# Performance work log

Hardware: AMD Instinct MI355X
Metric: run time of the kernel (lower is better)

## Reference

```python
import jax, jax.numpy as jnp
import numpy as np

B, S, D = 2, 1024, 1024
E, K, I = 8, 2, 1024
LIMIT = 7.0
ALPHA = 1.702


def setup_inputs() -> dict:
    key = jax.random.key(0)
    k0, k1, k2, k3 = jax.random.split(key, 4)
    return {
        "x": jax.random.normal(k0, (B, S, D), jnp.float32),
        "norm_w": jnp.ones((D,), jnp.float32),
        "gate_w": jax.random.normal(k1, (E, D), jnp.float32) / np.sqrt(D).astype(np.float32),
        "gate_b": jnp.zeros((E,), jnp.float32),
        "mlp1_w": jax.random.normal(k2, (E, 2 * I, D), jnp.float32) / np.sqrt(D).astype(np.float32),
        "mlp1_b": jnp.zeros((E, 2 * I), jnp.float32),
        "mlp2_w": jax.random.normal(k3, (E, D, I), jnp.float32) / np.sqrt(I).astype(np.float32),
        "mlp2_b": jnp.zeros((E, D), jnp.float32),
    }


def _swiglu(t, limit):
    # interleaved gate/linear split (gpt-oss style) with clamping
    glu = jnp.minimum(t[..., ::2], limit)
    lin = jnp.clip(t[..., 1::2], -limit, limit)
    return glu * jax.nn.sigmoid(ALPHA * glu) * (lin + 1.0)


def reference(x, norm_w, gate_w, gate_b, mlp1_w, mlp1_b, mlp2_w, mlp2_b):
    eps = jnp.finfo(x.dtype).eps
    # RMSNorm
    h = x * jax.lax.rsqrt(jnp.mean(x * x, axis=-1, keepdims=True) + eps) * norm_w
    flat = h.reshape(-1, D)                              # [T, D]
    # top-k gating
    logits = flat @ gate_w.T + gate_b                    # [T, E]
    vals, idx = jax.lax.top_k(logits, K)                 # sorted descending
    wts = jax.nn.softmax(vals, axis=-1)                  # [T, K]
    # per-expert SwiGLU MLP (dense over experts, identical math to per-token gather)
    t1 = jnp.einsum('td,efd->tef', flat, mlp1_w) + mlp1_b   # [T, E, 2I]
    act = _swiglu(t1, LIMIT)                                 # [T, E, I]
    y = jnp.einsum('tei,edi->ted', act, mlp2_w) + mlp2_b     # [T, E, D]
    # gather selected experts and combine
    sel = jnp.take_along_axis(y, idx[:, :, None], axis=1)    # [T, K, D]
    out = jnp.sum(sel * wts[:, :, None], axis=1).reshape(x.shape)
    return x + out
```

## Files before the change

kernel.cpp:

```cpp
#include <hip/hip_runtime.h>
#include <stdint.h>

#define TNUM 2048
#define DDIM 1024
#define NEXP 8
#define KSEL 2
#define IDIM 1024
#define TWOI 2048
#define LIMITV 7.0f
#define ALPHAV 1.702f
#define ROWT_MAX 40
#define RMSB (TNUM / 4)
#define N81 (NEXP * TWOI * DDIM / 8)
#define N82 (NEXP * DDIM * IDIM / 8)
#define G1TOT (ROWT_MAX * (TWOI / 128))
#define G2TOT (2 * ROWT_MAX * (DDIM / 128))

typedef __attribute__((ext_vector_type(8))) short bf16x8;
typedef __attribute__((ext_vector_type(4))) float f32x4;

#define VMCNT0() asm volatile("s_waitcnt vmcnt(0)" ::: "memory")
#define BARRIER() asm volatile("s_barrier" ::: "memory")

__device__ __forceinline__ unsigned short f2bf(float f) {
  unsigned u = __float_as_uint(f);
  u += 0x7FFF + ((u >> 16) & 1);
  return (unsigned short)(u >> 16);
}

__device__ __forceinline__ int4 cvt8(float4 a, float4 b) {
  union { unsigned short us[8]; int4 v; } o;
  o.us[0] = f2bf(a.x); o.us[1] = f2bf(a.y); o.us[2] = f2bf(a.z); o.us[3] = f2bf(a.w);
  o.us[4] = f2bf(b.x); o.us[5] = f2bf(b.y); o.us[6] = f2bf(b.z); o.us[7] = f2bf(b.w);
  return o.v;
}

__device__ __forceinline__ float4 ld4bf(const unsigned short* p) {
  int2 v = *(const int2*)p;
  unsigned a = (unsigned)v.x, b = (unsigned)v.y;
  float4 r;
  r.x = __uint_as_float((a & 0xFFFFu) << 16);
  r.y = __uint_as_float(a & 0xFFFF0000u);
  r.z = __uint_as_float((b & 0xFFFFu) << 16);
  r.w = __uint_as_float(b & 0xFFFF0000u);
  return r;
}

__device__ __forceinline__ void gl2lds16(const void* g, void* l) {
  __builtin_amdgcn_global_load_lds(
      (__attribute__((address_space(1))) unsigned int*)(uintptr_t)g,
      (__attribute__((address_space(3))) unsigned int*)(uintptr_t)l, 16, 0, 0);
}

__device__ __forceinline__ int xcd_swz(int bid, int total) {
  int q = total >> 3, r = total & 7;
  int xcd = bid & 7, pos = bid >> 3;
  return (xcd < r ? xcd * (q + 1) : r * (q + 1) + (xcd - r) * q) + pos;
}

__global__ __launch_bounds__(256) void k_rms_cvt(
    const float* __restrict__ x, const float* __restrict__ norm_w,
    const float* __restrict__ gate_w, const float* __restrict__ gate_b,
    const float* __restrict__ w1f, unsigned short* __restrict__ w1b,
    unsigned short* __restrict__ hb, int* __restrict__ tidx,
    float* __restrict__ twt) {
  if ((int)blockIdx.x >= RMSB) {
    int k0 = ((int)blockIdx.x - RMSB) * 1024 + (int)threadIdx.x;
    const float4* s = (const float4*)w1f;
#pragma unroll
    for (int i = 0; i < 4; ++i) {
      int k = k0 + i * 256;
      if (k < N81) ((int4*)w1b)[k] = cvt8(s[2 * k], s[2 * k + 1]);
    }
    return;
  }
  const int lane = threadIdx.x & 63;
  const int t = blockIdx.x * 4 + (threadIdx.x >> 6);

  const float4* xr  = (const float4*)x + (size_t)t * 256 + lane * 4;
  const float4* nwr = (const float4*)norm_w + lane * 4;
  const float4* gbr = (const float4*)gate_b;
  float4 xv[4], nwv[4];
#pragma unroll
  for (int i = 0; i < 4; ++i) xv[i] = xr[i];
  float4 gb0 = gbr[0], gb1 = gbr[1];
#pragma unroll
  for (int i = 0; i < 4; ++i) nwv[i] = nwr[i];

  float ss = 0.f;
#pragma unroll
  for (int i = 0; i < 4; ++i)
    ss += xv[i].x * xv[i].x + xv[i].y * xv[i].y + xv[i].z * xv[i].z + xv[i].w * xv[i].w;
#pragma unroll
  for (int m = 1; m < 64; m <<= 1) ss += __shfl_xor(ss, m);
  const float sc = rsqrtf(ss * (1.0f / DDIM) + 1.1920929e-07f);

  float4 h[4];
#pragma unroll
  for (int i = 0; i < 4; ++i) {
    h[i].x = xv[i].x * sc * nwv[i].x;
    h[i].y = xv[i].y * sc * nwv[i].y;
    h[i].z = xv[i].z * sc * nwv[i].z;
    h[i].w = xv[i].w * sc * nwv[i].w;
  }
  int4* hw = (int4*)(hb + (size_t)t * DDIM + lane * 16);
  hw[0] = cvt8(h[0], h[1]);
  hw[1] = cvt8(h[2], h[3]);

  float p[NEXP];
#pragma unroll
  for (int e = 0; e < NEXP; ++e) {
    const float4* g4 = (const float4*)gate_w + e * 256 + lane * 4;
    float4 a = g4[0], b = g4[1], c = g4[2], d = g4[3];
    p[e] = h[0].x * a.x + h[0].y * a.y + h[0].z * a.z + h[0].w * a.w
         + h[1].x * b.x + h[1].y * b.y + h[1].z * b.z + h[1].w * b.w
         + h[2].x * c.x + h[2].y * c.y + h[2].z * c.z + h[2].w * c.w
         + h[3].x * d.x + h[3].y * d.y + h[3].z * d.z + h[3].w * d.w;
  }
#pragma unroll
  for (int m = 1; m < 64; m <<= 1) {
#pragma unroll
    for (int e = 0; e < NEXP; ++e) p[e] += __shfl_xor(p[e], m);
  }
  p[0] += gb0.x; p[1] += gb0.y; p[2] += gb0.z; p[3] += gb0.w;
  p[4] += gb1.x; p[5] += gb1.y; p[6] += gb1.z; p[7] += gb1.w;

  if (lane == 0) {
    int i0 = 0; float v0 = p[0];
#pragma unroll
    for (int e = 1; e < NEXP; ++e) if (p[e] > v0) { v0 = p[e]; i0 = e; }
    int i1 = -1; float v1 = -3.4e38f;
#pragma unroll
    for (int e = 0; e < NEXP; ++e) if (e != i0 && p[e] > v1) { v1 = p[e]; i1 = e; }
    float e1 = __expf(v1 - v0);
    float w0 = 1.f / (1.f + e1);
    int2 ip; ip.x = i0; ip.y = i1;
    float2 wp; wp.x = w0; wp.y = e1 * w0;
    ((int2*)tidx)[t] = ip;
    ((float2*)twt)[t] = wp;
  }
}

__global__ __launch_bounds__(512) void k_sched(
    const int* __restrict__ tidx, int* __restrict__ meta,
    int* __restrict__ tl, int* __restrict__ rows, int* __restrict__ sof) {
  __shared__ unsigned short cnt[256][NEXP];
  __shared__ int off[NEXP];
  __shared__ int tot[NEXP];
  const int tid = threadIdx.x;
  int e_[16], rel_[16];
  if (tid < 256) {
#pragma unroll
    for (int k = 0; k < 16; ++k) e_[k] = tidx[tid * 16 + k];
#pragma unroll
    for (int k = 0; k < 16; ++k) {
      int r = 0;
#pragma unroll
      for (int j2 = 0; j2 < 16; ++j2)
        if (j2 < k) r += (e_[j2] == e_[k]) ? 1 : 0;
      rel_[k] = r;
    }
#pragma unroll
    for (int e = 0; e < NEXP; ++e) {
      int c = 0;
#pragma unroll
      for (int k = 0; k < 16; ++k) c += (e_[k] == e) ? 1 : 0;
      cnt[tid][e] = (unsigned short)c;
    }
  }
  __syncthreads();
  {
    const int we = tid >> 6, lane = tid & 63;
    int carry = 0;
#pragma unroll
    for (int chunk = 0; chunk < 4; ++chunk) {
      int i = chunk * 64 + lane;
      int c = (int)cnt[i][we];
      int s = c;
#pragma unroll
      for (int o = 1; o < 64; o <<= 1) {
        int t2 = __shfl_up(s, o);
        if (lane >= o) s += t2;
      }
      cnt[i][we] = (unsigned short)(s - c + carry);
      carry += __shfl(s, 63);
    }
    if (lane == 0) tot[we] = carry;
  }
  __syncthreads();
  if (tid == 0) {
    int acc = 0, nt = 0;
    for (int e = 0; e < NEXP; ++e) {
      meta[8 + e] = acc; off[e] = acc;
      int c = tot[e]; acc += c;
      int ntile = (c + 127) >> 7;
      for (int r = 0; r < ntile; ++r) tl[nt++] = (e << 8) | r;
    }
    meta[16] = acc;
    meta[25] = nt;
  }
  __syncthreads();
  if (tid < 256) {
#pragma unroll
    for (int k = 0; k < 16; ++k) {
      int i = tid * 16 + k;
      int e = e_[k];
      int slot = off[e] + (int)cnt[tid][e] + rel_[k];
      rows[slot] = i >> 1;
      sof[i] = slot;
    }
  }
}

__global__ __launch_bounds__(256, 4) void k_gemm1(
    const unsigned short* __restrict__ hb, const unsigned short* __restrict__ w1b,
    const float* __restrict__ mlp1_b, const int* __restrict__ meta,
    const int* __restrict__ tl, const int* __restrict__ rows,
    const float* __restrict__ w2f, unsigned short* __restrict__ w2b,
    unsigned short* __restrict__ actb) {
  const int bid = blockIdx.x;
  const int tid = threadIdx.x, lane = tid & 63, wid = tid >> 6;
  if (bid >= G1TOT) {
    int k0 = (bid - G1TOT) * 1024 + tid;
    const float4* s = (const float4*)w2f;
#pragma unroll
    for (int i = 0; i < 4; ++i) {
      int k = k0 + i * 256;
      if (k < N82) ((int4*)w2b)[k] = cvt8(s[2 * k], s[2 * k + 1]);
    }
    return;
  }
  const int nt = meta[25];
  const int total = nt * (TWOI / 128);
  if (bid >= total) return;
  const int j = xcd_swz(bid, total);
  const int ct = j / nt;
  const int tile = tl[j - ct * nt];
  const int e = tile >> 8, rt = tile & 255;
  const int offs = meta[8 + e];
  const int n_e = meta[9 + e] - offs;

  __shared__ unsigned short As[128][64];
  __shared__ unsigned short Bs[128][64];
  __shared__ int srow[128];
  if (tid < 128) srow[tid] = rows[offs + min(rt * 128 + tid, n_e - 1)];
  __syncthreads();

  const int rloc = tid >> 3;
  const int csw  = (((tid & 7) ^ (rloc & 7)) << 3);
  const unsigned short* gA[4];
  const unsigned short* gB[4];
  const unsigned short* w1e = w1b + (size_t)e * TWOI * DDIM;
#pragma unroll
  for (int jj = 0; jj < 4; ++jj) {
    gA[jj] = hb + (size_t)srow[jj * 32 + rloc] * DDIM + csw;
    gB[jj] = w1e + (size_t)(ct * 128 + jj * 32 + rloc) * DDIM + csw;
  }

#define G1_STAGE(KT)                                                           \
  _Pragma("unroll") for (int jj = 0; jj < 4; ++jj) {                           \
    gl2lds16(gA[jj] + (KT) * 64, &As[0][0] + jj * 2048 + tid * 8);             \
    gl2lds16(gB[jj] + (KT) * 64, &Bs[0][0] + jj * 2048 + tid * 8);             \
  }

  f32x4 acc[4][4];
#pragma unroll
  for (int m = 0; m < 4; ++m)
#pragma unroll
    for (int n = 0; n < 4; ++n) acc[m][n] = (f32x4){0.f, 0.f, 0.f, 0.f};

  const int wr = wid >> 1, wc = wid & 1;
  const int lrow = lane & 15, ksub = (lane >> 4) * 8;
  const int NK = DDIM / 64;

#pragma unroll
  for (int kt = 0; kt < NK; ++kt) {
    G1_STAGE(kt)
    VMCNT0();
    BARRIER();
#pragma unroll
    for (int kk = 0; kk < 2; ++kk) {
      bf16x8 af[4], bfr[4];
#pragma unroll
      for (int m = 0; m < 4; ++m) {
        int row = wr * 64 + m * 16 + lrow;
        int chunk = ((kk * 32 + ksub) >> 3) ^ (row & 7);
        af[m] = *(const bf16x8*)&As[row][chunk * 8];
      }
#pragma unroll
      for (int n = 0; n < 4; ++n) {
        int row = wc * 64 + n * 16 + lrow;
        int chunk = ((kk * 32 + ksub) >> 3) ^ (row & 7);
        bfr[n] = *(const bf16x8*)&Bs[row][chunk * 8];
      }
#pragma unroll
      for (int m = 0; m < 4; ++m)
#pragma unroll
        for (int n = 0; n < 4; ++n)
          acc[m][n] = __builtin_amdgcn_mfma_f32_16x16x32_bf16(af[m], bfr[n], acc[m][n], 0, 0, 0);
    }
    BARRIER();
  }
#undef G1_STAGE

  const float* b1e = mlp1_b + e * TWOI;
#pragma unroll
  for (int m = 0; m < 4; ++m) {
#pragma unroll
    for (int n = 0; n < 4; ++n) {
      int cg = ct * 128 + wc * 64 + n * 16 + (lane & 15);
      float bias = b1e[cg];
#pragma unroll
      for (int j2 = 0; j2 < 4; ++j2) {
        float val = acc[m][n][j2] + bias;
        float part = __shfl_xor(val, 1);
        int rl = wr * 64 + m * 16 + ((lane >> 4) << 2) + j2;
        if (!(lane & 1)) {
          float glu = fminf(val, LIMITV);
          float lin = fminf(fmaxf(part, -LIMITV), LIMITV);
          float s = 1.f / (1.f + __expf(-ALPHAV * glu));
          float a = glu * s * (lin + 1.f);
          if (rt * 128 + rl < n_e)
            actb[(size_t)(offs + rt * 128 + rl) * IDIM + (cg >> 1)] = f2bf(a);
        }
      }
    }
  }
}

__global__ __launch_bounds__(256, 4) void k_gemm2(
    const unsigned short* __restrict__ actb, const unsigned short* __restrict__ w2b,
    const float* __restrict__ mlp2_b, const int* __restrict__ meta,
    const int* __restrict__ tl, unsigned short* __restrict__ ybuf) {
  const int nt = meta[25];
  const int totalK = nt * (DDIM / 128) * 2;
  const int bid = blockIdx.x;
  if (bid >= totalK) return;
  const int j = xcd_swz(bid, totalK);
  const int kp = j & 1;
  const int jt = j >> 1;
  const int ct = jt / nt;
  const int tile = tl[jt - ct * nt];
  const int e = tile >> 8, rt = tile & 255;
  const int offs = meta[8 + e];
  const int n_e = meta[9 + e] - offs;
  const int tid = threadIdx.x, lane = tid & 63, wid = tid >> 6;

  __shared__ unsigned short As[128][64];
  __shared__ unsigned short Bs[128][64];

  const int rloc = tid >> 3;
  const int csw  = (((tid & 7) ^ (rloc & 7)) << 3);
  const int koff = kp * 512;
  const unsigned short* gA[4];
  const unsigned short* gB[4];
  const unsigned short* w2e = w2b + (size_t)e * DDIM * IDIM;
#pragma unroll
  for (int jj = 0; jj < 4; ++jj) {
    gA[jj] = actb + (size_t)(offs + min(rt * 128 + jj * 32 + rloc, n_e - 1)) * IDIM + koff + csw;
    gB[jj] = w2e + (size_t)(ct * 128 + jj * 32 + rloc) * IDIM + koff + csw;
  }

#define G2_STAGE(KT)                                                           \
  _Pragma("unroll") for (int jj = 0; jj < 4; ++jj) {                           \
    gl2lds16(gA[jj] + (KT) * 64, &As[0][0] + jj * 2048 + tid * 8);             \
    gl2lds16(gB[jj] + (KT) * 64, &Bs[0][0] + jj * 2048 + tid * 8);             \
  }

  f32x4 acc[4][4];
#pragma unroll
  for (int m = 0; m < 4; ++m)
#pragma unroll
    for (int n = 0; n < 4; ++n) acc[m][n] = (f32x4){0.f, 0.f, 0.f, 0.f};

  const int wr = wid >> 1, wc = wid & 1;
  const int lrow = lane & 15, ksub = (lane >> 4) * 8;
  const int NK = 512 / 64;

#pragma unroll
  for (int kt = 0; kt < NK; ++kt) {
    G2_STAGE(kt)
    VMCNT0();
    BARRIER();
#pragma unroll
    for (int kk = 0; kk < 2; ++kk) {
      bf16x8 af[4], bfr[4];
#pragma unroll
      for (int m = 0; m < 4; ++m) {
        int row = wr * 64 + m * 16 + lrow;
        int chunk = ((kk * 32 + ksub) >> 3) ^ (row & 7);
        af[m] = *(const bf16x8*)&As[row][chunk * 8];
      }
#pragma unroll
      for (int n = 0; n < 4; ++n) {
        int row = wc * 64 + n * 16 + lrow;
        int chunk = ((kk * 32 + ksub) >> 3) ^ (row & 7);
        bfr[n] = *(const bf16x8*)&Bs[row][chunk * 8];
      }
#pragma unroll
      for (int m = 0; m < 4; ++m)
#pragma unroll
        for (int n = 0; n < 4; ++n)
          acc[m][n] = __builtin_amdgcn_mfma_f32_16x16x32_bf16(af[m], bfr[n], acc[m][n], 0, 0, 0);
    }
    BARRIER();
  }
#undef G2_STAGE

  const float* b2e = mlp2_b + e * DDIM;
  unsigned short* yh = ybuf + (size_t)kp * TNUM * KSEL * DDIM;
#pragma unroll
  for (int m = 0; m < 4; ++m) {
#pragma unroll
    for (int n = 0; n < 4; ++n) {
      int d = ct * 128 + wc * 64 + n * 16 + (lane & 15);
      float bias = kp ? 0.f : b2e[d];
#pragma unroll
      for (int j2 = 0; j2 < 4; ++j2) {
        int rl = wr * 64 + m * 16 + ((lane >> 4) << 2) + j2;
        if (rt * 128 + rl < n_e)
          yh[(size_t)(offs + rt * 128 + rl) * DDIM + d] = f2bf(acc[m][n][j2] + bias);
      }
    }
  }
}

__global__ __launch_bounds__(256) void k_combine(
    const float* __restrict__ x, const unsigned short* __restrict__ ybuf,
    const int* __restrict__ sof, const float* __restrict__ twt,
    float* __restrict__ out) {
  int t = blockIdx.x, tid = threadIdx.x;
  int s0 = sof[2 * t], s1 = sof[2 * t + 1];
  float w0 = twt[2 * t], w1 = twt[2 * t + 1];
  const size_t H = (size_t)TNUM * KSEL * DDIM;
  float4 xv = ((const float4*)x)[t * 256 + tid];
  float4 a0 = ld4bf(ybuf + (size_t)s0 * DDIM + tid * 4);
  float4 a1 = ld4bf(ybuf + H + (size_t)s0 * DDIM + tid * 4);
  float4 b0 = ld4bf(ybuf + (size_t)s1 * DDIM + tid * 4);
  float4 b1 = ld4bf(ybuf + H + (size_t)s1 * DDIM + tid * 4);
  float4 o;
  o.x = xv.x + w0 * (a0.x + a1.x) + w1 * (b0.x + b1.x);
  o.y = xv.y + w0 * (a0.y + a1.y) + w1 * (b0.y + b1.y);
  o.z = xv.z + w0 * (a0.z + a1.z) + w1 * (b0.z + b1.z);
  o.w = xv.w + w0 * (a0.w + a1.w) + w1 * (b0.w + b1.w);
  ((float4*)out)[t * 256 + tid] = o;
}

extern "C" void kernel_launch(void* const* d_in, const int* in_sizes, int n_in,
                              void* d_out, int out_size, void* d_ws, size_t ws_size,
                              hipStream_t stream) {
  const float* x      = (const float*)d_in[0];
  const float* norm_w = (const float*)d_in[1];
  const float* gate_w = (const float*)d_in[2];
  const float* gate_b = (const float*)d_in[3];
  const float* mlp1_w = (const float*)d_in[4];
  const float* mlp1_b = (const float*)d_in[5];
  const float* mlp2_w = (const float*)d_in[6];
  const float* mlp2_b = (const float*)d_in[7];
  float* out = (float*)d_out;

  char* w = (char*)d_ws;
  unsigned short* w1b = (unsigned short*)w; w += (size_t)NEXP * TWOI * DDIM * 2;
  unsigned short* w2b = (unsigned short*)w; w += (size_t)NEXP * DDIM * IDIM * 2;
  unsigned short* hb  = (unsigned short*)w; w += (size_t)TNUM * DDIM * 2;
  unsigned short* actb = (unsigned short*)w; w += (size_t)TNUM * KSEL * IDIM * 2;
  unsigned short* ybuf = (unsigned short*)w; w += (size_t)2 * TNUM * KSEL * DDIM * 2;
  int*   tidx = (int*)w;  w += TNUM * KSEL * 4;
  float* twt  = (float*)w; w += TNUM * KSEL * 4;
  int*   sof  = (int*)w;  w += TNUM * KSEL * 4;
  int*   rows = (int*)w;  w += TNUM * KSEL * 4;
  int*   meta = (int*)w;  w += 32 * 4;
  int*   tl   = (int*)w;  w += 64 * 4;

  k_rms_cvt<<<RMSB + N81 / 1024, 256, 0, stream>>>(x, norm_w, gate_w, gate_b,
                                                   mlp1_w, w1b, hb, tidx, twt);
  k_sched<<<1, 512, 0, stream>>>(tidx, meta, tl, rows, sof);
  k_gemm1<<<G1TOT + N82 / 1024, 256, 0, stream>>>(hb, w1b, mlp1_b, meta, tl, rows,
                                                  mlp2_w, w2b, actb);
  k_gemm2<<<G2TOT, 256, 0, stream>>>(actb, w2b, mlp2_b, meta, tl, ybuf);
  k_combine<<<TNUM, 256, 0, stream>>>(x, ybuf, sof, twt, out);
}
```

Before: 100.3 us.

## Split GEMM1 over K into two halves and move SwiGLU to a separate kernel

GEMM1 is now split-K by two, so each block handles half the reduction dimension and writes bf16 partial sums to a scratch buffer. A new k_swiglu kernel sums the two partials, adds the bias and applies the clamped SwiGLU to produce the activations. The aim is to double the number of GEMM1 blocks and raise GPU occupancy. In exchange it adds an extra kernel launch, extra global-memory round trips for the partials, and a bf16 rounding step before the bias and activation. The partial buffer shares workspace with ybuf.

```diff
diff --git a/kernel.cpp b/kernel.cpp
--- a/kernel.cpp
+++ b/kernel.cpp
@@ -13,8 +13,9 @@
 #define RMSB (TNUM / 4)
 #define N81 (NEXP * TWOI * DDIM / 8)
 #define N82 (NEXP * DDIM * IDIM / 8)
-#define G1TOT (ROWT_MAX * (TWOI / 128))
+#define G1K (2 * ROWT_MAX * (TWOI / 128))
 #define G2TOT (2 * ROWT_MAX * (DDIM / 128))
+#define NSLOT (TNUM * KSEL)
 
 typedef __attribute__((ext_vector_type(8))) short bf16x8;
 typedef __attribute__((ext_vector_type(4))) float f32x4;
@@ -26,6 +27,10 @@
   unsigned u = __float_as_uint(f);
   u += 0x7FFF + ((u >> 16) & 1);
   return (unsigned short)(u >> 16);
+}
+
+__device__ __forceinline__ float bf2f(unsigned short v) {
+  return __uint_as_float((unsigned)v << 16);
 }
 
 __device__ __forceinline__ int4 cvt8(float4 a, float4 b) {
@@ -214,14 +219,14 @@
 
 __global__ __launch_bounds__(256, 4) void k_gemm1(
     const unsigned short* __restrict__ hb, const unsigned short* __restrict__ w1b,
-    const float* __restrict__ mlp1_b, const int* __restrict__ meta,
-    const int* __restrict__ tl, const int* __restrict__ rows,
+    const int* __restrict__ meta, const int* __restrict__ tl,
+    const int* __restrict__ rows,
     const float* __restrict__ w2f, unsigned short* __restrict__ w2b,
-    unsigned short* __restrict__ actb) {
+    unsigned short* __restrict__ p1buf) {
   const int bid = blockIdx.x;
   const int tid = threadIdx.x, lane = tid & 63, wid = tid >> 6;
-  if (bid >= G1TOT) {
-    int k0 = (bid - G1TOT) * 1024 + tid;
+  if (bid >= G1K) {
+    int k0 = (bid - G1K) * 1024 + tid;
     const float4* s = (const float4*)w2f;
 #pragma unroll
     for (int i = 0; i < 4; ++i) {
@@ -231,11 +236,13 @@
     return;
   }
   const int nt = meta[25];
-  const int total = nt * (TWOI / 128);
-  if (bid >= total) return;
-  const int j = xcd_swz(bid, total);
-  const int ct = j / nt;
-  const int tile = tl[j - ct * nt];
+  const int totalK = nt * (TWOI / 128) * 2;
+  if (bid >= totalK) return;
+  const int j = xcd_swz(bid, totalK);
+  const int kp = j & 1;
+  const int jt = j >> 1;
+  const int ct = jt / nt;
+  const int tile = tl[jt - ct * nt];
   const int e = tile >> 8, rt = tile & 255;
   const int offs = meta[8 + e];
   const int n_e = meta[9 + e] - offs;
@@ -248,13 +255,14 @@
 
   const int rloc = tid >> 3;
   const int csw  = (((tid & 7) ^ (rloc & 7)) << 3);
+  const int koff = kp * 512;
   const unsigned short* gA[4];
   const unsigned short* gB[4];
   const unsigned short* w1e = w1b + (size_t)e * TWOI * DDIM;
 #pragma unroll
   for (int jj = 0; jj < 4; ++jj) {
-    gA[jj] = hb + (size_t)srow[jj * 32 + rloc] * DDIM + csw;
-    gB[jj] = w1e + (size_t)(ct * 128 + jj * 32 + rloc) * DDIM + csw;
+    gA[jj] = hb + (size_t)srow[jj * 32 + rloc] * DDIM + koff + csw;
+    gB[jj] = w1e + (size_t)(ct * 128 + jj * 32 + rloc) * DDIM + koff + csw;
   }
 
 #define G1_STAGE(KT)                                                           \
@@ -271,7 +279,7 @@
 
   const int wr = wid >> 1, wc = wid & 1;
   const int lrow = lane & 15, ksub = (lane >> 4) * 8;
-  const int NK = DDIM / 64;
+  const int NK = 512 / 64;
 
 #pragma unroll
   for (int kt = 0; kt < NK; ++kt) {
@@ -303,29 +311,54 @@
   }
 #undef G1_STAGE
 
-  const float* b1e = mlp1_b + e * TWOI;
+  unsigned short* ph = p1buf + (size_t)kp * NSLOT * TWOI;
 #pragma unroll
   for (int m = 0; m < 4; ++m) {
 #pragma unroll
     for (int n = 0; n < 4; ++n) {
       int cg = ct * 128 + wc * 64 + n * 16 + (lane & 15);
-      float bias = b1e[cg];
 #pragma unroll
       for (int j2 = 0; j2 < 4; ++j2) {
-        float val = acc[m][n][j2] + bias;
-        float part = __shfl_xor(val, 1);
         int rl = wr * 64 + m * 16 + ((lane >> 4) << 2) + j2;
-        if (!(lane & 1)) {
-          float glu = fminf(val, LIMITV);
-          float lin = fminf(fmaxf(part, -LIMITV), LIMITV);
-          float s = 1.f / (1.f + __expf(-ALPHAV * glu));
-          float a = glu * s * (lin + 1.f);
-          if (rt * 128 + rl < n_e)
-            actb[(size_t)(offs + rt * 128 + rl) * IDIM + (cg >> 1)] = f2bf(a);
-        }
-      }
-    }
-  }
+        if (rt * 128 + rl < n_e)
+          ph[(size_t)(offs + rt * 128 + rl) * TWOI + cg] = f2bf(acc[m][n][j2]);
+      }
+    }
+  }
+}
+
+__global__ __launch_bounds__(256) void k_swiglu(
+    const unsigned short* __restrict__ p1buf, const float* __restrict__ mlp1_b,
+    const int* __restrict__ meta, unsigned short* __restrict__ actb) {
+  const int slot = blockIdx.x, tid = threadIdx.x;
+  int e = 0;
+#pragma unroll
+  for (int i = 1; i < NEXP; ++i) e += (slot >= meta[8 + i]) ? 1 : 0;
+  const float* b1e = mlp1_b + e * TWOI;
+
+  const size_t H = (size_t)NSLOT * TWOI;
+  const int cg0 = tid * 8;
+  const unsigned short* p0 = p1buf + (size_t)slot * TWOI + cg0;
+  float4 a0 = ld4bf(p0), a1 = ld4bf(p0 + 4);
+  float4 b0 = ld4bf(p0 + H), b1 = ld4bf(p0 + H + 4);
+  const float4* bb = (const float4*)(b1e + cg0);
+  float4 c0 = bb[0], c1 = bb[1];
+
+  float t[8];
+  t[0] = a0.x + b0.x + c0.x; t[1] = a0.y + b0.y + c0.y;
+  t[2] = a0.z + b0.z + c0.z; t[3] = a0.w + b0.w + c0.w;
+  t[4] = a1.x + b1.x + c1.x; t[5] = a1.y + b1.y + c1.y;
+  t[6] = a1.z + b1.z + c1.z; t[7] = a1.w + b1.w + c1.w;
+
+  union { unsigned short us[4]; int2 v; } o;
+#pragma unroll
+  for (int i = 0; i < 4; ++i) {
+    float glu = fminf(t[2 * i], LIMITV);
+    float lin = fminf(fmaxf(t[2 * i + 1], -LIMITV), LIMITV);
+    float s = 1.f / (1.f + __expf(-ALPHAV * glu));
+    o.us[i] = f2bf(glu * s * (lin + 1.f));
+  }
+  ((int2*)(actb + (size_t)slot * IDIM + (cg0 >> 1)))[0] = o.v;
 }
 
 __global__ __launch_bounds__(256, 4) void k_gemm2(
@@ -408,7 +441,7 @@
 #undef G2_STAGE
 
   const float* b2e = mlp2_b + e * DDIM;
-  unsigned short* yh = ybuf + (size_t)kp * TNUM * KSEL * DDIM;
+  unsigned short* yh = ybuf + (size_t)kp * NSLOT * DDIM;
 #pragma unroll
   for (int m = 0; m < 4; ++m) {
 #pragma unroll
@@ -432,7 +465,7 @@
   int t = blockIdx.x, tid = threadIdx.x;
   int s0 = sof[2 * t], s1 = sof[2 * t + 1];
   float w0 = twt[2 * t], w1 = twt[2 * t + 1];
-  const size_t H = (size_t)TNUM * KSEL * DDIM;
+  const size_t H = (size_t)NSLOT * DDIM;
   float4 xv = ((const float4*)x)[t * 256 + tid];
   float4 a0 = ld4bf(ybuf + (size_t)s0 * DDIM + tid * 4);
   float4 a1 = ld4bf(ybuf + H + (size_t)s0 * DDIM + tid * 4);
@@ -463,8 +496,10 @@
   unsigned short* w1b = (unsigned short*)w; w += (size_t)NEXP * TWOI * DDIM * 2;
   unsigned short* w2b = (unsigned short*)w; w += (size_t)NEXP * DDIM * IDIM * 2;
   unsigned short* hb  = (unsigned short*)w; w += (size_t)TNUM * DDIM * 2;
-  unsigned short* actb = (unsigned short*)w; w += (size_t)TNUM * KSEL * IDIM * 2;
-  unsigned short* ybuf = (unsigned short*)w; w += (size_t)2 * TNUM * KSEL * DDIM * 2;
+  unsigned short* actb = (unsigned short*)w; w += (size_t)NSLOT * IDIM * 2;
+  unsigned short* p1buf = (unsigned short*)w;
+  unsigned short* ybuf  = (unsigned short*)w;
+  w += (size_t)2 * NSLOT * TWOI * 2;
   int*   tidx = (int*)w;  w += TNUM * KSEL * 4;
   float* twt  = (float*)w; w += TNUM * KSEL * 4;
   int*   sof  = (int*)w;  w += TNUM * KSEL * 4;
@@ -475,8 +510,9 @@
   k_rms_cvt<<<RMSB + N81 / 1024, 256, 0, stream>>>(x, norm_w, gate_w, gate_b,
                                                    mlp1_w, w1b, hb, tidx, twt);
   k_sched<<<1, 512, 0, stream>>>(tidx, meta, tl, rows, sof);
-  k_gemm1<<<G1TOT + N82 / 1024, 256, 0, stream>>>(hb, w1b, mlp1_b, meta, tl, rows,
-                                                  mlp2_w, w2b, actb);
+  k_gemm1<<<G1K + N82 / 1024, 256, 0, stream>>>(hb, w1b, meta, tl, rows,
+                                                mlp2_w, w2b, p1buf);
+  k_swiglu<<<NSLOT, 256, 0, stream>>>(p1buf, mlp1_b, meta, actb);
   k_gemm2<<<G2TOT, 256, 0, stream>>>(actb, w2b, mlp2_b, meta, tl, ybuf);
   k_combine<<<TNUM, 256, 0, stream>>>(x, ybuf, sof, twt, out);
 }
```

New measurement: 114.5 us. 14.2% more time.
